# Kernel tuning notes

Measured on AMD Instinct MI355X. Metric: run time of the kernel, lower is better.

The kernel has to match this reference:

```python
import jax, jax.numpy as jnp
import numpy as np

MINVAL = 0.0
MAXVAL = 1.0
G = 4096   # grid_dim
C = 8      # channels
N = 4      # batch


def setup_inputs() -> dict:
    key = jax.random.key(0)
    k1, k2 = jax.random.split(key)
    # uniform 1-D grid on [0, 1) -> dx = 1/G (get_dx(grid))
    grid = jnp.arange(G, dtype=jnp.float32) / G
    density = jax.random.normal(k1, (N, 1, G), dtype=jnp.float32)
    # nn.Parameter xi initialized with nn.init.uniform_ -> U[0, 1)
    xi = jax.random.uniform(k2, (C,), dtype=jnp.float32)
    return {"density": density, "xi": xi, "grid": grid}


def reference(density, xi, grid):
    # density: (N, 1, G); xi: (C,); grid: (G,)
    dx = grid[1] - grid[0]                                   # uniform spacing
    g = jnp.abs(grid[:, None] - grid[None, :])               # (G, G) pairwise |x_i - x_j|
    xi_eff = 1.0 / (MINVAL + (MAXVAL - MINVAL) * jax.nn.sigmoid(xi))  # (C,)
    expo = jnp.exp(-g[None, :, :] * xi_eff[:, None, None])   # (C, G, G) dense kernel
    # 'i, jkl, ilm -> jim': sum over singleton channel k of density and grid dim l
    integral = jnp.einsum('i,jkl,ilm->jim', 0.5 * xi_eff, density, expo)  # (N, C, G)
    return integral * dx
```

## Files before the change

### kernel.cpp

```cpp
#include <hip/hip_runtime.h>


#define GG 4096
#define CC 8
#define NN 4
#define BLOCK 256
#define CHUNK (GG / BLOCK)

__global__ __launch_bounds__(BLOCK) void gconv_scan(const float* __restrict__ density,
                                                    const float* __restrict__ xi,
                                                    const float* __restrict__ grid,
                                                    float* __restrict__ out) {
    const int bid  = blockIdx.x;
    const int c    = bid & (CC - 1);
    const int n    = bid >> 3;
    const int tid  = threadIdx.x;
    const int base = tid * CHUNK;

    const float k  = 1.0f + expf(-xi[c]);
    const float dx = grid[1] - grid[0];

    const float4* dv4 = reinterpret_cast<const float4*>(density + n * GG + base);
    const float4* gv4 = reinterpret_cast<const float4*>(grid + base);

    float ea[CHUNK];
    float eb[CHUNK];
    float pa[CHUNK];
    float sb[CHUNK];

    float runA = 0.0f;
#pragma unroll
    for (int q = 0; q < CHUNK / 4; ++q) {
        float4 d4 = dv4[q];
        float4 g4 = gv4[q];
        float xs[4] = {g4.x, g4.y, g4.z, g4.w};
        float ds[4] = {d4.x, d4.y, d4.z, d4.w};
#pragma unroll
        for (int j = 0; j < 4; ++j) {
            const int i = q * 4 + j;
            const float e  = expf(xs[j] * k);
            const float ei = expf(-xs[j] * k);
            ea[i] = e;
            eb[i] = ei;
            runA += ds[j] * e;
            pa[i] = runA;
            sb[i] = ds[j] * ei;
        }
    }
    float runB = 0.0f;
#pragma unroll
    for (int i = CHUNK - 1; i >= 0; --i) {
        const float bv = sb[i];
        sb[i] = runB;
        runB += bv;
    }

    float sA = runA, sB = runB;
#pragma unroll
    for (int off = 1; off < 64; off <<= 1) {
        const float tA = __shfl_up(sA, off, 64);
        const float tB = __shfl_up(sB, off, 64);
        if ((tid & 63) >= off) { sA += tA; sB += tB; }
    }

    __shared__ float wA[BLOCK / 64];
    __shared__ float wB[BLOCK / 64];
    const int wave = tid >> 6;
    if ((tid & 63) == 63) { wA[wave] = sA; wB[wave] = sB; }
    __syncthreads();

    float preA = 0.0f, preB = 0.0f, totB = 0.0f;
#pragma unroll
    for (int w = 0; w < BLOCK / 64; ++w) {
        const float ta = wA[w];
        const float tb = wB[w];
        if (w < wave) { preA += ta; preB += tb; }
        totB += tb;
    }
    const float offA = preA + (sA - runA);
    const float offB = totB - (preB + sB);

    const float scale = 0.5f * k * dx;
    float4* o4 = reinterpret_cast<float4*>(out + bid * GG + base);
#pragma unroll
    for (int q = 0; q < CHUNK / 4; ++q) {
        float4 r;
        float* rp = &r.x;
#pragma unroll
        for (int j = 0; j < 4; ++j) {
            const int i = q * 4 + j;
            const float A = offA + pa[i];
            const float B = offB + sb[i];
            rp[j] = scale * (eb[i] * A + ea[i] * B);
        }
        o4[q] = r;
    }
}

extern "C" void kernel_launch(void* const* d_in, const int* in_sizes, int n_in,
                              void* d_out, int out_size, void* d_ws, size_t ws_size,
                              hipStream_t stream) {
    const float* density = (const float*)d_in[0];
    const float* xi      = (const float*)d_in[1];
    const float* grid    = (const float*)d_in[2];
    float* out           = (float*)d_out;

    gconv_scan<<<NN * CC, BLOCK, 0, stream>>>(density, xi, grid, out);
}
```

Baseline: 59.14 us.

## Split scan into segment-partials and finalize kernels across many more blocks

Replaces the single 32-block scan kernel with two kernels launched over 512 blocks. The first computes per-segment totals of density*exp(±kx) into workspace, and the second redoes the exponentials, performs an intra-segment scan and adds the cross-segment offsets. It also switches to fast __expf intrinsics. This is meant to raise parallelism on a device with many compute units, at the cost of an extra launch, recomputation and a small workspace round trip.

```diff
diff --git a/kernel.cpp b/kernel.cpp
--- a/kernel.cpp
+++ b/kernel.cpp
@@ -4,65 +4,78 @@
 #define GG 4096
 #define CC 8
 #define NN 4
+#define SS 16
+#define SEG (GG / SS)
 #define BLOCK 256
-#define CHUNK (GG / BLOCK)
 
-__global__ __launch_bounds__(BLOCK) void gconv_scan(const float* __restrict__ density,
-                                                    const float* __restrict__ xi,
-                                                    const float* __restrict__ grid,
-                                                    float* __restrict__ out) {
-    const int bid  = blockIdx.x;
-    const int c    = bid & (CC - 1);
-    const int n    = bid >> 3;
-    const int tid  = threadIdx.x;
-    const int base = tid * CHUNK;
 
-    const float k  = 1.0f + expf(-xi[c]);
-    const float dx = grid[1] - grid[0];
+__global__ __launch_bounds__(BLOCK) void gconv_partials(const float* __restrict__ density,
+                                                        const float* __restrict__ xi,
+                                                        const float* __restrict__ grid,
+                                                        float* __restrict__ ws) {
+    const int bid = blockIdx.x;
+    const int s   = bid & (SS - 1);
+    const int c   = (bid >> 4) & (CC - 1);
+    const int n   = bid >> 7;
+    const int tid = threadIdx.x;
+    const int m   = s * SEG + tid;
 
-    const float4* dv4 = reinterpret_cast<const float4*>(density + n * GG + base);
-    const float4* gv4 = reinterpret_cast<const float4*>(grid + base);
+    const float k  = 1.0f + __expf(-xi[c]);
+    const float x  = grid[m];
+    const float d  = density[n * GG + m];
+    const float ea = __expf(x * k);
+    const float eb = __expf(-x * k);
+    float a = d * ea;
+    float b = d * eb;
 
-    float ea[CHUNK];
-    float eb[CHUNK];
-    float pa[CHUNK];
-    float sb[CHUNK];
-
-    float runA = 0.0f;
 #pragma unroll
-    for (int q = 0; q < CHUNK / 4; ++q) {
-        float4 d4 = dv4[q];
-        float4 g4 = gv4[q];
-        float xs[4] = {g4.x, g4.y, g4.z, g4.w};
-        float ds[4] = {d4.x, d4.y, d4.z, d4.w};
-#pragma unroll
-        for (int j = 0; j < 4; ++j) {
-            const int i = q * 4 + j;
-            const float e  = expf(xs[j] * k);
-            const float ei = expf(-xs[j] * k);
-            ea[i] = e;
-            eb[i] = ei;
-            runA += ds[j] * e;
-            pa[i] = runA;
-            sb[i] = ds[j] * ei;
-        }
-    }
-    float runB = 0.0f;
-#pragma unroll
-    for (int i = CHUNK - 1; i >= 0; --i) {
-        const float bv = sb[i];
-        sb[i] = runB;
-        runB += bv;
+    for (int off = 32; off >= 1; off >>= 1) {
+        a += __shfl_xor(a, off, 64);
+        b += __shfl_xor(b, off, 64);
     }
 
-    float sA = runA, sB = runB;
+    __shared__ float lA[BLOCK / 64];
+    __shared__ float lB[BLOCK / 64];
+    const int wave = tid >> 6;
+    if ((tid & 63) == 0) { lA[wave] = a; lB[wave] = b; }
+    __syncthreads();
+    if (tid == 0) {
+        float tA = 0.0f, tB = 0.0f;
+#pragma unroll
+        for (int w = 0; w < BLOCK / 64; ++w) { tA += lA[w]; tB += lB[w]; }
+        ws[bid] = tA;
+        ws[NN * CC * SS + bid] = tB;
+    }
+}
+
+__global__ __launch_bounds__(BLOCK) void gconv_finalize(const float* __restrict__ density,
+                                                        const float* __restrict__ xi,
+                                                        const float* __restrict__ grid,
+                                                        const float* __restrict__ ws,
+                                                        float* __restrict__ out) {
+    const int bid = blockIdx.x;
+    const int s   = bid & (SS - 1);
+    const int c   = (bid >> 4) & (CC - 1);
+    const int n   = bid >> 7;
+    const int tid = threadIdx.x;
+    const int m   = s * SEG + tid;
+
+    const float k  = 1.0f + __expf(-xi[c]);
+    const float dx = grid[1] - grid[0];
+    const float x  = grid[m];
+    const float d  = density[n * GG + m];
+    const float ea = __expf(x * k);
+    const float eb = __expf(-x * k);
+    const float a = d * ea;
+    const float b = d * eb;
+
+    float sA = a, sB = b;
 #pragma unroll
     for (int off = 1; off < 64; off <<= 1) {
         const float tA = __shfl_up(sA, off, 64);
         const float tB = __shfl_up(sB, off, 64);
         if ((tid & 63) >= off) { sA += tA; sB += tB; }
     }
-
     __shared__ float wA[BLOCK / 64];
     __shared__ float wB[BLOCK / 64];
     const int wave = tid >> 6;
@@ -77,24 +90,22 @@
         if (w < wave) { preA += ta; preB += tb; }
         totB += tb;
     }
-    const float offA = preA + (sA - runA);
-    const float offB = totB - (preB + sB);
+    const float pA   = preA + sA;
+    const float sufB = totB - (preB + sB);
+
+    const float* __restrict__ sumA = ws + (bid - s);
+    const float* __restrict__ sumB = ws + NN * CC * SS + (bid - s);
+    float offA = 0.0f, offB = 0.0f;
+#pragma unroll
+    for (int sp = 0; sp < SS; ++sp) {
+        const float vA = sumA[sp];
+        const float vB = sumB[sp];
+        if (sp < s) offA += vA;
+        if (sp > s) offB += vB;
+    }
 
     const float scale = 0.5f * k * dx;
-    float4* o4 = reinterpret_cast<float4*>(out + bid * GG + base);
-#pragma unroll
-    for (int q = 0; q < CHUNK / 4; ++q) {
-        float4 r;
-        float* rp = &r.x;
-#pragma unroll
-        for (int j = 0; j < 4; ++j) {
-            const int i = q * 4 + j;
-            const float A = offA + pa[i];
-            const float B = offB + sb[i];
-            rp[j] = scale * (eb[i] * A + ea[i] * B);
-        }
-        o4[q] = r;
-    }
+    out[(n * CC + c) * GG + m] = scale * (eb * (offA + pA) + ea * (offB + sufB));
 }
 
 extern "C" void kernel_launch(void* const* d_in, const int* in_sizes, int n_in,
@@ -104,6 +115,8 @@
     const float* xi      = (const float*)d_in[1];
     const float* grid    = (const float*)d_in[2];
     float* out           = (float*)d_out;
+    float* ws            = (float*)d_ws;
 
-    gconv_scan<<<NN * CC, BLOCK, 0, stream>>>(density, xi, grid, out);
+    gconv_partials<<<NN * CC * SS, BLOCK, 0, stream>>>(density, xi, grid, ws);
+    gconv_finalize<<<NN * CC * SS, BLOCK, 0, stream>>>(density, xi, grid, ws, out);
 }
```

Result: no change. 59.58 us (+0.7%).
